# Optimization experiments

Hardware: AMD Instinct MI355X
Metric: run time of the kernel (lower is better)

The kernel has to match this reference:

```python
import jax, jax.numpy as jnp
import numpy as np

B, S, H, L, A, V, NL = 16, 256, 768, 12, 12, 30522, 9
DH = H // A
FF = 4 * H


def _ln(x, g, b):
    m = x.mean(-1, keepdims=True)
    v = jnp.var(x, axis=-1, keepdims=True)
    return (x - m) * jax.lax.rsqrt(v + 1e-12) * g + b


def setup_inputs() -> dict:
    key = jax.random.key(0)
    ks = jax.random.split(key, 16)
    n = lambda k, shape: jax.random.normal(k, shape, jnp.float32) * 0.02
    return {
        "input_word_ids": jax.random.randint(ks[0], (B, S), 0, V, jnp.int32),
        "input_mask": jnp.ones((B, S), jnp.int32),
        "input_type_ids": jnp.zeros((B, S), jnp.int32),
        "valid_mask": jax.random.randint(ks[1], (B, S), 0, 2, jnp.int32),
        "word_emb": n(ks[2], (V, H)),
        "pos_emb": n(ks[3], (S, H)),
        "type_emb": n(ks[4], (2, H)),
        "emb_ln_g": jnp.ones((H,), jnp.float32),
        "emb_ln_b": jnp.zeros((H,), jnp.float32),
        "Wq": n(ks[5], (L, H, H)), "bq": jnp.zeros((L, H), jnp.float32),
        "Wk": n(ks[6], (L, H, H)), "bk": jnp.zeros((L, H), jnp.float32),
        "Wv": n(ks[7], (L, H, H)), "bv": jnp.zeros((L, H), jnp.float32),
        "Wo": n(ks[8], (L, H, H)), "bo": jnp.zeros((L, H), jnp.float32),
        "attn_ln_g": jnp.ones((L, H), jnp.float32),
        "attn_ln_b": jnp.zeros((L, H), jnp.float32),
        "W1": n(ks[9], (L, H, FF)), "b1": jnp.zeros((L, FF), jnp.float32),
        "W2": n(ks[10], (L, FF, H)), "b2": jnp.zeros((L, H), jnp.float32),
        "ffn_ln_g": jnp.ones((L, H), jnp.float32),
        "ffn_ln_b": jnp.zeros((L, H), jnp.float32),
        "cls_W": n(ks[11], (H, NL)),
        "cls_b": jnp.zeros((NL,), jnp.float32),
    }


def reference(input_word_ids, input_mask, input_type_ids, valid_mask,
              word_emb, pos_emb, type_emb, emb_ln_g, emb_ln_b,
              Wq, bq, Wk, bk, Wv, bv, Wo, bo, attn_ln_g, attn_ln_b,
              W1, b1, W2, b2, ffn_ln_g, ffn_ln_b, cls_W, cls_b):
    # --- BERT embeddings ---
    x = word_emb[input_word_ids] + pos_emb[None, :, :] + type_emb[input_type_ids]
    x = _ln(x, emb_ln_g, emb_ln_b)
    amask = (1.0 - input_mask.astype(jnp.float32))[:, None, None, :] * -10000.0

    # --- 12 post-LN transformer layers via scan over stacked weights ---
    def block(x, p):
        wq, bq_, wk, bk_, wv, bv_, wo, bo_, ag, ab, w1, b1_, w2, b2_, fg, fb = p
        q = (x @ wq + bq_).reshape(B, S, A, DH)
        k = (x @ wk + bk_).reshape(B, S, A, DH)
        v = (x @ wv + bv_).reshape(B, S, A, DH)
        s = jnp.einsum('bqhd,bkhd->bhqk', q, k) * (1.0 / float(np.sqrt(DH))) + amask
        a = jax.nn.softmax(s, axis=-1)
        ctx = jnp.einsum('bhqk,bkhd->bqhd', a, v).reshape(B, S, H)
        x = _ln(x + ctx @ wo + bo_, ag, ab)
        h = jax.nn.gelu(x @ w1 + b1_)
        x = _ln(x + h @ w2 + b2_, fg, fb)
        return x, None

    x, _ = jax.lax.scan(block, x, (Wq, bq, Wk, bk, Wv, bv, Wo, bo,
                                   attn_ln_g, attn_ln_b, W1, b1, W2, b2,
                                   ffn_ln_g, ffn_ln_b))

    # --- valid-mask token compaction: valid tokens to front, zero pad ---
    # stable argsort moves valid_mask==1 positions to the front, in order
    order = jnp.argsort(1 - valid_mask, axis=1)  # stable by default
    gathered = jnp.take_along_axis(x, order[:, :, None], axis=1)
    counts = valid_mask.sum(axis=1)  # [B]
    keep = (jnp.arange(S)[None, :] < counts[:, None])[:, :, None]
    valid_out = jnp.where(keep, gathered, jnp.zeros((), x.dtype))

    # dropout is identity (training=False default); softmax classifier head
    return jax.nn.softmax(valid_out @ cls_W + cls_b, axis=-1)
```

## Files before the change

kernel.cpp:

```cpp
#include <hip/hip_runtime.h>

#define TOKENS 4096
#define BATCH  16
#define SEQ    256
#define Hdim   768
#define FFdim  3072
#define NHEAD  12
#define NLBL   9
#define NLAYER 12
#define QKVS   2304

typedef unsigned short u16;
typedef __attribute__((ext_vector_type(8))) short short8;
typedef __attribute__((ext_vector_type(4))) float floatx4;

__device__ __forceinline__ float bf2f(u16 u) {
    union { unsigned int i; float f; } c; c.i = ((unsigned int)u) << 16; return c.f;
}
__device__ __forceinline__ u16 f2bf(float f) {
    union { float f; unsigned int i; } c; c.f = f;
    unsigned int u = c.i;
    u = u + 0x7fffu + ((u >> 16) & 1u);
    return (u16)(u >> 16);
}

#define GLOAD16(gp, lp) __builtin_amdgcn_global_load_lds( \
    (__attribute__((address_space(1))) void*)(gp), \
    (__attribute__((address_space(3))) void*)(lp), 16, 0, 0)

__global__ __launch_bounds__(256) void k_conv_layer(
    const float* __restrict__ Wq, const float* __restrict__ Wk,
    const float* __restrict__ Wv, const float* __restrict__ Wo,
    const float* __restrict__ W1, const float* __restrict__ W2,
    u16* __restrict__ qkvT, u16* __restrict__ oT,
    u16* __restrict__ w1T, u16* __restrict__ w2T)
{
    int bid = blockIdx.x;
    const float* src; u16* dst; int K, N, t;
    if (bid < 576) {
        int m = bid / 144; t = bid - m * 144;
        src = (m == 0) ? Wq : (m == 1) ? Wk : (m == 2) ? Wv : Wo;
        dst = (m < 3) ? (qkvT + (size_t)m * 768 * 768) : oT;
        K = 768; N = 768;
    } else if (bid < 1152) {
        t = bid - 576; src = W1; dst = w1T; K = 768; N = 3072;
    } else {
        t = bid - 1152; src = W2; dst = w2T; K = 3072; N = 768;
    }
    int ntn = N >> 6;
    int tk = t / ntn, tn = t - tk * ntn;

    __shared__ float ld[64][65];
    int tid = threadIdx.x;
    int rr = tid >> 4;
    int cc = (tid & 15) * 4;
#pragma unroll
    for (int i = 0; i < 4; i++) {
        int k = tk * 64 + rr + i * 16;
        float4 v = *(const float4*)(src + (size_t)k * N + tn * 64 + cc);
        ld[rr + i * 16][cc + 0] = v.x;
        ld[rr + i * 16][cc + 1] = v.y;
        ld[rr + i * 16][cc + 2] = v.z;
        ld[rr + i * 16][cc + 3] = v.w;
    }
    __syncthreads();
    int n  = tid >> 2;
    int kc = (tid & 3) * 16;
    union { u16 h[16]; uint4 v[2]; } ob;
#pragma unroll
    for (int j = 0; j < 16; j++) ob.h[j] = f2bf(ld[kc + j][n]);
    u16* op = dst + (size_t)(tn * 64 + n) * K + tk * 64 + kc;
    *(uint4*)(op)     = ob.v[0];
    *(uint4*)(op + 8) = ob.v[1];
}

__global__ void k_biascat(const float* __restrict__ bq, const float* __restrict__ bk,
                          const float* __restrict__ bv, float* __restrict__ o)
{
    int l = blockIdx.x, t = threadIdx.x;
    o[l * QKVS + t]        = bq[l * Hdim + t];
    o[l * QKVS + 768 + t]  = bk[l * Hdim + t];
    o[l * QKVS + 1536 + t] = bv[l * Hdim + t];
}

template<int MODE>
__global__ __launch_bounds__(256) void k_gemm(const u16* __restrict__ Ag, const u16* __restrict__ Bg,
                                              const float* __restrict__ bias, void* __restrict__ outp,
                                              int N, int K)
{
    __shared__ u16 As[128 * 32];
    __shared__ u16 Bs[128 * 32];
    const int tid  = threadIdx.x;
    const int lane = tid & 63, w = tid >> 6;
    const int wr = w >> 1, wc = w & 1;
    const int quad = lane >> 4, l16 = lane & 15;
    const int m0 = blockIdx.y * 128, n0 = blockIdx.x * 128;

    const int r0 = tid >> 2, c0 = (tid & 3) * 8;
    const u16* a0 = Ag + (size_t)(m0 + r0) * K + c0;
    const u16* a1 = Ag + (size_t)(m0 + 64 + r0) * K + c0;
    const u16* b0 = Bg + (size_t)(n0 + r0) * K + c0;
    const u16* b1 = Bg + (size_t)(n0 + 64 + r0) * K + c0;
    u16* as0 = As + (size_t)(w * 64) * 8;
    u16* as1 = As + (size_t)(256 + w * 64) * 8;
    u16* bs0 = Bs + (size_t)(w * 64) * 8;
    u16* bs1 = Bs + (size_t)(256 + w * 64) * 8;

    const floatx4 vzero = {0.f, 0.f, 0.f, 0.f};
    floatx4 acc[4][4];
#pragma unroll
    for (int i = 0; i < 4; i++)
#pragma unroll
        for (int j = 0; j < 4; j++) acc[i][j] = vzero;

    for (int k0 = 0; k0 < K; k0 += 32) {
        GLOAD16(a0 + k0, as0);
        GLOAD16(a1 + k0, as1);
        GLOAD16(b0 + k0, bs0);
        GLOAD16(b1 + k0, bs1);
        __syncthreads();
        short8 af[4], bfr[4];
#pragma unroll
        for (int mt = 0; mt < 4; mt++) af[mt]  = *(const short8*)(&As[(wr * 64 + mt * 16 + l16) * 32 + quad * 8]);
#pragma unroll
        for (int nt = 0; nt < 4; nt++) bfr[nt] = *(const short8*)(&Bs[(wc * 64 + nt * 16 + l16) * 32 + quad * 8]);
#pragma unroll
        for (int mt = 0; mt < 4; mt++)
#pragma unroll
            for (int nt = 0; nt < 4; nt++)
                acc[mt][nt] = __builtin_amdgcn_mfma_f32_16x16x32_bf16(af[mt], bfr[nt], acc[mt][nt], 0, 0, 0);
        __syncthreads();
    }
#pragma unroll
    for (int mt = 0; mt < 4; mt++) {
#pragma unroll
        for (int nt = 0; nt < 4; nt++) {
            int col = n0 + wc * 64 + nt * 16 + l16;
            float bv = bias[col];
#pragma unroll
            for (int r = 0; r < 4; r++) {
                int row = m0 + wr * 64 + mt * 16 + quad * 4 + r;
                float vv = acc[mt][nt][r] + bv;
                if (MODE == 1) {
                    float t = 0.7978845608028654f * (vv + 0.044715f * vv * vv * vv);
                    vv = 0.5f * vv * (1.0f + tanhf(t));
                }
                if (MODE == 2) ((float*)outp)[(size_t)row * N + col] = vv;
                else          ((u16*)outp)[(size_t)row * N + col] = f2bf(vv);
            }
        }
    }
}

__global__ __launch_bounds__(256) void k_embed(const int* __restrict__ wid, const int* __restrict__ tidv,
                                               const float* __restrict__ we, const float* __restrict__ pe, const float* __restrict__ te,
                                               const float* __restrict__ g, const float* __restrict__ bb,
                                               float* __restrict__ xf, u16* __restrict__ xh)
{
    int i = blockIdx.x; int s = i & 255;
    int t = threadIdx.x;
    int wv = wid[i], tv = tidv[i];
    float e[3]; float sum = 0.f, sq = 0.f;
#pragma unroll
    for (int r = 0; r < 3; r++) {
        int j = t + r * 256;
        float x = we[(size_t)wv * Hdim + j] + pe[s * Hdim + j] + te[tv * Hdim + j];
        e[r] = x; sum += x; sq += x * x;
    }
    __shared__ float red[8];
    for (int off = 32; off; off >>= 1) { sum += __shfl_xor(sum, off); sq += __shfl_xor(sq, off); }
    if ((t & 63) == 0) { red[t >> 6] = sum; red[4 + (t >> 6)] = sq; }
    __syncthreads();
    sum = red[0] + red[1] + red[2] + red[3];
    sq  = red[4] + red[5] + red[6] + red[7];
    float mean = sum * (1.0f / Hdim);
    float var  = sq * (1.0f / Hdim) - mean * mean;
    float rstd = rsqrtf(var + 1e-12f);
#pragma unroll
    for (int r = 0; r < 3; r++) {
        int j = t + r * 256;
        float v = (e[r] - mean) * rstd * g[j] + bb[j];
        xf[(size_t)i * Hdim + j] = v;
        xh[(size_t)i * Hdim + j] = f2bf(v);
    }
}

__global__ __launch_bounds__(256) void k_addln(float* __restrict__ xf, const float* __restrict__ y,
                                               const float* __restrict__ g, const float* __restrict__ bb,
                                               u16* __restrict__ xh)
{
    int i = blockIdx.x; int t = threadIdx.x;
    float e[3]; float sum = 0.f, sq = 0.f;
#pragma unroll
    for (int r = 0; r < 3; r++) {
        int j = t + r * 256;
        float x = xf[(size_t)i * Hdim + j] + y[(size_t)i * Hdim + j];
        e[r] = x; sum += x; sq += x * x;
    }
    __shared__ float red[8];
    for (int off = 32; off; off >>= 1) { sum += __shfl_xor(sum, off); sq += __shfl_xor(sq, off); }
    if ((t & 63) == 0) { red[t >> 6] = sum; red[4 + (t >> 6)] = sq; }
    __syncthreads();
    sum = red[0] + red[1] + red[2] + red[3];
    sq  = red[4] + red[5] + red[6] + red[7];
    float mean = sum * (1.0f / Hdim);
    float var  = sq * (1.0f / Hdim) - mean * mean;
    float rstd = rsqrtf(var + 1e-12f);
#pragma unroll
    for (int r = 0; r < 3; r++) {
        int j = t + r * 256;
        float v = (e[r] - mean) * rstd * g[j] + bb[j];
        xf[(size_t)i * Hdim + j] = v;
        xh[(size_t)i * Hdim + j] = f2bf(v);
    }
}

__global__ __launch_bounds__(256, 2) void k_attn(const u16* __restrict__ qkv, const int* __restrict__ maskg,
                                                 u16* __restrict__ ctx)
{
    __shared__ u16 Vt[64 * 264];
    __shared__ u16 Ps[4 * 64 * 40];
    __shared__ float madd[256];
    int bh = blockIdx.x; int b = bh / NHEAD; int h = bh - b * NHEAD;
    int tid = threadIdx.x; int lane = tid & 63; int w = tid >> 6;
    int quad = lane >> 4, l16 = lane & 15;
    size_t baseq = (size_t)b * SEQ * QKVS + h * 64;
    size_t basec = (size_t)b * SEQ * Hdim + h * 64;

#pragma unroll
    for (int i = 0; i < 8; i++) {
        int c = tid + i * 256; int key = c >> 3; int cc = (c & 7) << 3;
        uint4 vv = *(const uint4*)(qkv + baseq + 1536 + (size_t)key * QKVS + cc);
        const u16* p16 = (const u16*)&vv;
#pragma unroll
        for (int e = 0; e < 8; e++) Vt[(cc + e) * 264 + key] = p16[e];
    }
    madd[tid] = (1.0f - (float)maskg[b * SEQ + tid]) * -10000.0f;
    __syncthreads();

    short8 aq[4][2];
#pragma unroll
    for (int mt = 0; mt < 4; mt++)
#pragma unroll
        for (int kf = 0; kf < 2; kf++)
            aq[mt][kf] = *(const short8*)(qkv + baseq + (size_t)(w * 64 + mt * 16 + l16) * QKVS + kf * 32 + quad * 8);

    const floatx4 vzero = {0.f, 0.f, 0.f, 0.f};
    floatx4 acc[4][4];
    float l_run[4][4];
#pragma unroll
    for (int a = 0; a < 4; a++)
#pragma unroll
        for (int r = 0; r < 4; r++) { acc[a][r] = vzero; l_run[a][r] = 0.f; }

    u16* Pw = &Ps[w * 64 * 40];

    for (int kc = 0; kc < 8; kc++) {
        floatx4 sc[4][2];
#pragma unroll
        for (int mt = 0; mt < 4; mt++) { sc[mt][0] = vzero; sc[mt][1] = vzero; }
#pragma unroll
        for (int kf = 0; kf < 2; kf++) {
            short8 bk_[2];
#pragma unroll
            for (int nt = 0; nt < 2; nt++)
                bk_[nt] = *(const short8*)(qkv + baseq + 768 + (size_t)(kc * 32 + nt * 16 + l16) * QKVS + kf * 32 + quad * 8);
#pragma unroll
            for (int mt = 0; mt < 4; mt++)
#pragma unroll
                for (int nt = 0; nt < 2; nt++)
                    sc[mt][nt] = __builtin_amdgcn_mfma_f32_16x16x32_bf16(aq[mt][kf], bk_[nt], sc[mt][nt], 0, 0, 0);
        }
        float madd0 = madd[kc * 32 + l16];
        float madd1 = madd[kc * 32 + 16 + l16];
#pragma unroll
        for (int mt = 0; mt < 4; mt++) {
#pragma unroll
            for (int r = 0; r < 4; r++) {
                float p0 = __expf(sc[mt][0][r] * 0.125f + madd0);
                float p1 = __expf(sc[mt][1][r] * 0.125f + madd1);
                float ls = p0 + p1;
#pragma unroll
                for (int off = 1; off < 16; off <<= 1) ls += __shfl_xor(ls, off);
                l_run[mt][r] += ls;
                int row = mt * 16 + quad * 4 + r;
                Pw[row * 40 + l16]      = f2bf(p0);
                Pw[row * 40 + 16 + l16] = f2bf(p1);
            }
        }
        short8 ap[4], bv_[4];
#pragma unroll
        for (int nt = 0; nt < 4; nt++)
            bv_[nt] = *(const short8*)(&Vt[(nt * 16 + l16) * 264 + kc * 32 + quad * 8]);
#pragma unroll
        for (int mt = 0; mt < 4; mt++)
            ap[mt] = *(const short8*)(&Pw[(mt * 16 + l16) * 40 + quad * 8]);
#pragma unroll
        for (int mt = 0; mt < 4; mt++)
#pragma unroll
            for (int nt = 0; nt < 4; nt++)
                acc[mt][nt] = __builtin_amdgcn_mfma_f32_16x16x32_bf16(ap[mt], bv_[nt], acc[mt][nt], 0, 0, 0);
    }
#pragma unroll
    for (int mt = 0; mt < 4; mt++)
#pragma unroll
        for (int r = 0; r < 4; r++) {
            float inv = 1.0f / l_run[mt][r];
            int sq_ = w * 64 + mt * 16 + quad * 4 + r;
#pragma unroll
            for (int nt = 0; nt < 4; nt++)
                ctx[basec + (size_t)sq_ * Hdim + nt * 16 + l16] = f2bf(acc[mt][nt][r] * inv);
        }
}

__global__ void k_compact(const int* __restrict__ vm, int* __restrict__ counts, int* __restrict__ srcidx)
{
    int b = blockIdx.x;
    if (threadIdx.x == 0) {
        int c = 0;
        for (int s = 0; s < SEQ; s++)
            if (vm[b * SEQ + s]) { srcidx[b * SEQ + c] = s; c++; }
        counts[b] = c;
    }
}

__global__ __launch_bounds__(256) void k_cls(const u16* __restrict__ x, const int* __restrict__ counts,
                                             const int* __restrict__ srcidx, const float* __restrict__ Wc,
                                             const float* __restrict__ bc, float* __restrict__ out)
{
    int w = threadIdx.x >> 6, lane = threadIdx.x & 63;
    int row = blockIdx.x * 4 + w;
    int b = row >> 8, s = row & 255;
    float acc[NLBL];
#pragma unroll
    for (int n = 0; n < NLBL; n++) acc[n] = 0.f;
    int cnt = counts[b];
    if (s < cnt) {
        int src = srcidx[b * SEQ + s];
        const u16* xr = x + (size_t)(b * SEQ + src) * Hdim;
        for (int j = lane; j < Hdim; j += 64) {
            float xv = bf2f(xr[j]);
#pragma unroll
            for (int n = 0; n < NLBL; n++) acc[n] += xv * Wc[j * NLBL + n];
        }
    }
#pragma unroll
    for (int n = 0; n < NLBL; n++)
        for (int off = 32; off; off >>= 1) acc[n] += __shfl_xor(acc[n], off);
    if (lane == 0) {
        float lg[NLBL]; float mx = -1e30f;
#pragma unroll
        for (int n = 0; n < NLBL; n++) { lg[n] = acc[n] + bc[n]; mx = fmaxf(mx, lg[n]); }
        float se = 0.f;
#pragma unroll
        for (int n = 0; n < NLBL; n++) { lg[n] = __expf(lg[n] - mx); se += lg[n]; }
        float inv = 1.0f / se;
#pragma unroll
        for (int n = 0; n < NLBL; n++) out[(size_t)row * NLBL + n] = lg[n] * inv;
    }
}

extern "C" void kernel_launch(void* const* d_in, const int* in_sizes, int n_in,
                              void* d_out, int out_size, void* d_ws, size_t ws_size,
                              hipStream_t stream)
{
    (void)in_sizes; (void)n_in; (void)out_size; (void)ws_size;
    const int* word_ids = (const int*)d_in[0];
    const int* in_mask  = (const int*)d_in[1];
    const int* type_ids = (const int*)d_in[2];
    const int* valid    = (const int*)d_in[3];
    const float* word_emb = (const float*)d_in[4];
    const float* pos_emb  = (const float*)d_in[5];
    const float* type_emb = (const float*)d_in[6];
    const float* eg = (const float*)d_in[7];
    const float* eb = (const float*)d_in[8];
    const float* Wq = (const float*)d_in[9];  const float* bq = (const float*)d_in[10];
    const float* Wk = (const float*)d_in[11]; const float* bk = (const float*)d_in[12];
    const float* Wv = (const float*)d_in[13]; const float* bv = (const float*)d_in[14];
    const float* Wo = (const float*)d_in[15]; const float* bo = (const float*)d_in[16];
    const float* ag = (const float*)d_in[17]; const float* ab = (const float*)d_in[18];
    const float* W1 = (const float*)d_in[19]; const float* b1 = (const float*)d_in[20];
    const float* W2 = (const float*)d_in[21]; const float* b2 = (const float*)d_in[22];
    const float* fg = (const float*)d_in[23]; const float* fb = (const float*)d_in[24];
    const float* Wc = (const float*)d_in[25]; const float* bc = (const float*)d_in[26];
    float* out = (float*)d_out;

    char* p = (char*)d_ws;
    int* counts = (int*)p;
    int* srcidx = (int*)(p + 1024);
    p += 65536;
    float* x_f32 = (float*)p; p += (size_t)TOKENS * Hdim * 4;
    u16* x_h  = (u16*)p; p += (size_t)TOKENS * Hdim * 2;
    float* tmpf = (float*)p; p += (size_t)TOKENS * Hdim * 4;
    u16* qkv_h = (u16*)p; p += (size_t)TOKENS * QKVS * 2;
    u16* c_h  = (u16*)p; p += (size_t)TOKENS * Hdim * 2;
    u16* h_h  = qkv_h;
    u16* wqkvT = (u16*)p; p += (size_t)QKVS * Hdim * 2;
    u16* woT   = (u16*)p; p += (size_t)Hdim * Hdim * 2;
    u16* w1T   = (u16*)p; p += (size_t)FFdim * Hdim * 2;
    u16* w2T   = (u16*)p; p += (size_t)Hdim * FFdim * 2;
    float* bqkv = (float*)p; p += (size_t)NLAYER * QKVS * 4;

    k_embed<<<TOKENS, 256, 0, stream>>>(word_ids, type_ids, word_emb, pos_emb, type_emb, eg, eb, x_f32, x_h);
    k_compact<<<BATCH, 64, 0, stream>>>(valid, counts, srcidx);
    k_biascat<<<NLAYER, 768, 0, stream>>>(bq, bk, bv, bqkv);

    for (int l = 0; l < NLAYER; l++) {
        size_t HH = (size_t)Hdim * Hdim;
        size_t HF = (size_t)Hdim * FFdim;
        k_conv_layer<<<1728, 256, 0, stream>>>(Wq + l * HH, Wk + l * HH, Wv + l * HH, Wo + l * HH,
                                               W1 + l * HF, W2 + l * HF, wqkvT, woT, w1T, w2T);
        k_gemm<0><<<dim3(18, 32), 256, 0, stream>>>(x_h, wqkvT, bqkv + l * QKVS, qkv_h, QKVS, Hdim);
        k_attn<<<BATCH * NHEAD, 256, 0, stream>>>(qkv_h, in_mask, c_h);
        k_gemm<2><<<dim3(6, 32), 256, 0, stream>>>(c_h, woT, bo + l * Hdim, tmpf, Hdim, Hdim);
        k_addln<<<TOKENS, 256, 0, stream>>>(x_f32, tmpf, ag + l * Hdim, ab + l * Hdim, x_h);
        k_gemm<1><<<dim3(24, 32), 256, 0, stream>>>(x_h, w1T, b1 + l * FFdim, h_h, FFdim, Hdim);
        k_gemm<2><<<dim3(6, 32), 256, 0, stream>>>(h_h, w2T, b2 + l * Hdim, tmpf, Hdim, FFdim);
        k_addln<<<TOKENS, 256, 0, stream>>>(x_f32, tmpf, fg + l * Hdim, fb + l * Hdim, x_h);
    }
    k_cls<<<TOKENS / 4, 256, 0, stream>>>(x_h, counts, srcidx, Wc, bc, out);
}
```

Baseline: 2.865 ms.

## Double-buffer GEMM LDS tiles and use narrower N tiles for H-output GEMMs

The GEMM kernel now keeps two LDS buffers and issues the global-to-LDS loads for the next K step before computing the current one. It uses explicit vmcnt waits and raw barriers so memory latency overlaps the MFMA work. A BN template parameter is added, and the N=768 GEMMs (output projection and FFN down-projection) switch to 64-wide tiles, doubling their grid to 384 blocks for better CU occupancy. The cost is twice the shared memory per block and more A-tile reloads for the narrow-tile GEMMs.

```diff
diff --git a/kernel.cpp b/kernel.cpp
--- a/kernel.cpp
+++ b/kernel.cpp
@@ -83,59 +83,85 @@
     o[l * QKVS + 1536 + t] = bv[l * Hdim + t];
 }
 
-template<int MODE>
+template<int MODE, int BN>
 __global__ __launch_bounds__(256) void k_gemm(const u16* __restrict__ Ag, const u16* __restrict__ Bg,
                                               const float* __restrict__ bias, void* __restrict__ outp,
                                               int N, int K)
 {
-    __shared__ u16 As[128 * 32];
-    __shared__ u16 Bs[128 * 32];
+    constexpr int NFR = BN / 32;
+    __shared__ u16 As[2][128 * 32];
+    __shared__ u16 Bs[2][BN * 32];
     const int tid  = threadIdx.x;
     const int lane = tid & 63, w = tid >> 6;
     const int wr = w >> 1, wc = w & 1;
     const int quad = lane >> 4, l16 = lane & 15;
-    const int m0 = blockIdx.y * 128, n0 = blockIdx.x * 128;
+    const int m0 = blockIdx.y * 128, n0 = blockIdx.x * BN;
 
     const int r0 = tid >> 2, c0 = (tid & 3) * 8;
     const u16* a0 = Ag + (size_t)(m0 + r0) * K + c0;
-    const u16* a1 = Ag + (size_t)(m0 + 64 + r0) * K + c0;
+    const u16* a1 = a0 + (size_t)64 * K;
     const u16* b0 = Bg + (size_t)(n0 + r0) * K + c0;
-    const u16* b1 = Bg + (size_t)(n0 + 64 + r0) * K + c0;
-    u16* as0 = As + (size_t)(w * 64) * 8;
-    u16* as1 = As + (size_t)(256 + w * 64) * 8;
-    u16* bs0 = Bs + (size_t)(w * 64) * 8;
-    u16* bs1 = Bs + (size_t)(256 + w * 64) * 8;
+    const u16* b1 = b0 + (size_t)64 * K;
+    const int lofs0 = w * 512;
+    const int lofs1 = 2048 + w * 512;
 
     const floatx4 vzero = {0.f, 0.f, 0.f, 0.f};
-    floatx4 acc[4][4];
+    floatx4 acc[4][NFR];
 #pragma unroll
     for (int i = 0; i < 4; i++)
 #pragma unroll
-        for (int j = 0; j < 4; j++) acc[i][j] = vzero;
-
-    for (int k0 = 0; k0 < K; k0 += 32) {
-        GLOAD16(a0 + k0, as0);
-        GLOAD16(a1 + k0, as1);
-        GLOAD16(b0 + k0, bs0);
-        GLOAD16(b1 + k0, bs1);
-        __syncthreads();
-        short8 af[4], bfr[4];
-#pragma unroll
-        for (int mt = 0; mt < 4; mt++) af[mt]  = *(const short8*)(&As[(wr * 64 + mt * 16 + l16) * 32 + quad * 8]);
-#pragma unroll
-        for (int nt = 0; nt < 4; nt++) bfr[nt] = *(const short8*)(&Bs[(wc * 64 + nt * 16 + l16) * 32 + quad * 8]);
+        for (int j = 0; j < NFR; j++) acc[i][j] = vzero;
+
+    const int NT = K >> 5;
+
+    GLOAD16(a0, &As[0][lofs0]);
+    GLOAD16(a1, &As[0][lofs1]);
+    GLOAD16(b0, &Bs[0][lofs0]);
+    if constexpr (BN == 128) GLOAD16(b1, &Bs[0][lofs1]);
+
+    for (int t = 0; t < NT; t++) {
+        const int cur = t & 1, nxt = cur ^ 1;
+        if (t + 1 < NT) {
+            const int k1 = (t + 1) << 5;
+            GLOAD16(a0 + k1, &As[nxt][lofs0]);
+            GLOAD16(a1 + k1, &As[nxt][lofs1]);
+            GLOAD16(b0 + k1, &Bs[nxt][lofs0]);
+            if constexpr (BN == 128) {
+                GLOAD16(b1 + k1, &Bs[nxt][lofs1]);
+                asm volatile("s_waitcnt vmcnt(4)" ::: "memory");
+            } else {
+                asm volatile("s_waitcnt vmcnt(3)" ::: "memory");
+            }
+        } else {
+            asm volatile("s_waitcnt vmcnt(0)" ::: "memory");
+        }
+        __builtin_amdgcn_sched_barrier(0);
+        __builtin_amdgcn_s_barrier();
+        __builtin_amdgcn_sched_barrier(0);
+
+        short8 af[4], bfr[NFR];
 #pragma unroll
         for (int mt = 0; mt < 4; mt++)
-#pragma unroll
-            for (int nt = 0; nt < 4; nt++)
+            af[mt]  = *(const short8*)(&As[cur][(wr * 64 + mt * 16 + l16) * 32 + quad * 8]);
+#pragma unroll
+        for (int nt = 0; nt < NFR; nt++)
+            bfr[nt] = *(const short8*)(&Bs[cur][(wc * (BN / 2) + nt * 16 + l16) * 32 + quad * 8]);
+#pragma unroll
+        for (int mt = 0; mt < 4; mt++)
+#pragma unroll
+            for (int nt = 0; nt < NFR; nt++)
                 acc[mt][nt] = __builtin_amdgcn_mfma_f32_16x16x32_bf16(af[mt], bfr[nt], acc[mt][nt], 0, 0, 0);
-        __syncthreads();
-    }
+
+        __builtin_amdgcn_sched_barrier(0);
+        __builtin_amdgcn_s_barrier();
+        __builtin_amdgcn_sched_barrier(0);
+    }
+
 #pragma unroll
     for (int mt = 0; mt < 4; mt++) {
 #pragma unroll
-        for (int nt = 0; nt < 4; nt++) {
-            int col = n0 + wc * 64 + nt * 16 + l16;
+        for (int nt = 0; nt < NFR; nt++) {
+            int col = n0 + wc * (BN / 2) + nt * 16 + l16;
             float bv = bias[col];
 #pragma unroll
             for (int r = 0; r < 4; r++) {
@@ -410,12 +436,12 @@
         size_t HF = (size_t)Hdim * FFdim;
         k_conv_layer<<<1728, 256, 0, stream>>>(Wq + l * HH, Wk + l * HH, Wv + l * HH, Wo + l * HH,
                                                W1 + l * HF, W2 + l * HF, wqkvT, woT, w1T, w2T);
-        k_gemm<0><<<dim3(18, 32), 256, 0, stream>>>(x_h, wqkvT, bqkv + l * QKVS, qkv_h, QKVS, Hdim);
+        k_gemm<0, 128><<<dim3(18, 32), 256, 0, stream>>>(x_h, wqkvT, bqkv + l * QKVS, qkv_h, QKVS, Hdim);
         k_attn<<<BATCH * NHEAD, 256, 0, stream>>>(qkv_h, in_mask, c_h);
-        k_gemm<2><<<dim3(6, 32), 256, 0, stream>>>(c_h, woT, bo + l * Hdim, tmpf, Hdim, Hdim);
+        k_gemm<2, 64><<<dim3(12, 32), 256, 0, stream>>>(c_h, woT, bo + l * Hdim, tmpf, Hdim, Hdim);
         k_addln<<<TOKENS, 256, 0, stream>>>(x_f32, tmpf, ag + l * Hdim, ab + l * Hdim, x_h);
-        k_gemm<1><<<dim3(24, 32), 256, 0, stream>>>(x_h, w1T, b1 + l * FFdim, h_h, FFdim, Hdim);
-        k_gemm<2><<<dim3(6, 32), 256, 0, stream>>>(h_h, w2T, b2 + l * Hdim, tmpf, Hdim, FFdim);
+        k_gemm<1, 128><<<dim3(24, 32), 256, 0, stream>>>(x_h, w1T, b1 + l * FFdim, h_h, FFdim, Hdim);
+        k_gemm<2, 64><<<dim3(12, 32), 256, 0, stream>>>(h_h, w2T, b2 + l * Hdim, tmpf, Hdim, FFdim);
         k_addln<<<TOKENS, 256, 0, stream>>>(x_f32, tmpf, fg + l * Hdim, fb + l * Hdim, x_h);
     }
     k_cls<<<TOKENS / 4, 256, 0, stream>>>(x_h, counts, srcidx, Wc, bc, out);
```

After: 2.597 ms. 9.4% less time.
